# Optimization experiments

Measured on AMD Instinct MI355X. Metric: run time of the kernel, lower is better.

Reference implementation:

```python
import jax, jax.numpy as jnp
import numpy as np
import math

H = 8  # num_heads
SCALE = 1.0 / math.sqrt(512.0)  # original divides by sqrt(dim_V), not sqrt(head_dim)


def setup_inputs() -> dict:
    key = jax.random.key(0)
    ks = jax.random.split(key, 16)
    B, N, D = 32, 512, 512
    s = 1.0 / math.sqrt(D)
    return {
        "Q": jax.random.normal(ks[0], (B, N, D), jnp.float32),
        "K": jax.random.normal(ks[1], (B, N, D), jnp.float32),
        "Wq": jax.random.normal(ks[2], (D, D), jnp.float32) * s,
        "bq": jnp.zeros((D,), jnp.float32),
        "Wk": jax.random.normal(ks[3], (D, D), jnp.float32) * s,
        "bk": jnp.zeros((D,), jnp.float32),
        "Wv": jax.random.normal(ks[4], (D, D), jnp.float32) * s,
        "bv": jnp.zeros((D,), jnp.float32),
        "Wo": jax.random.normal(ks[5], (D, D), jnp.float32) * s,
        "bo": jnp.zeros((D,), jnp.float32),
        "W1": jax.random.normal(ks[6], (D, D), jnp.float32) * s,
        "b1": jnp.zeros((D,), jnp.float32),
        "W2": jax.random.normal(ks[7], (D, D), jnp.float32) * s,
        "b2": jnp.zeros((D,), jnp.float32),
    }


def reference(Q, K, Wq, bq, Wk, bk, Wv, bv, Wo, bo, W1, b1, W2, b2):
    B, Nq, D = Q.shape
    dh = D // H
    # projections (torch Linear: x @ W.T + b)
    q = (Q @ Wq.T + bq).reshape(B, Nq, H, dh)
    k = (K @ Wk.T + bk).reshape(B, K.shape[1], H, dh)
    v = (K @ Wv.T + bv).reshape(B, K.shape[1], H, dh)
    # scores: [B, H, Nq, Nk], scaled by 1/sqrt(dim_V)
    scores = jnp.einsum("bqhd,bkhd->bhqk", q, k) * SCALE
    # NOTE: original softmax is over dim=1 of [H*B, Nq, Nk] == the QUERY axis
    A = jax.nn.softmax(scores, axis=2)
    attn = jnp.einsum("bhqk,bkhd->bqhd", A, v).reshape(B, Nq, D)
    out = Q + (attn @ Wo.T + bo)  # dropout p=0.0
    ffn = jax.nn.relu(out @ W1.T + b1) @ W2.T + b2
    return out + ffn
```

## Files before the change

kernel.cpp:

```cpp
#include <hip/hip_runtime.h>
#include <stdint.h>

#define SCALE_ 0.044194173824159216f

typedef __attribute__((ext_vector_type(8))) short bf16x8;
typedef __attribute__((ext_vector_type(4))) float f32x4;

__device__ __forceinline__ ushort f2b(float f) {
  union { float f; uint32_t u; } v; v.f = f;
  return (ushort)((v.u + 0x7fffu + ((v.u >> 16) & 1u)) >> 16);
}
__device__ __forceinline__ uint32_t cvtpk(float lo, float hi) {
  uint32_t r; asm("v_cvt_pk_bf16_f32 %0, %1, %2" : "=v"(r) : "v"(lo), "v"(hi)); return r;
}
__device__ __forceinline__ void gld16(void* lds, const void* g) {
  __builtin_amdgcn_global_load_lds(
      (const __attribute__((address_space(1))) uint32_t*)g,
      (__attribute__((address_space(3))) uint32_t*)lds, 16, 0, 0);
}

__global__ __launch_bounds__(256)
void k_cvt(const float* __restrict__ Q, const float* __restrict__ K,
           const float* __restrict__ w0, const float* __restrict__ w1,
           const float* __restrict__ w2, const float* __restrict__ w3,
           const float* __restrict__ w4, const float* __restrict__ w5,
           ushort* __restrict__ Qb, ushort* __restrict__ Kb, ushort* __restrict__ Wb)
{
  const long long NQ = 8388608LL, NW = 262144LL;
  long long i = ((long long)blockIdx.x * 256 + threadIdx.x) * 4;
  const float* src; ushort* dst; long long off;
  if (i < NQ)        { src = Q; dst = Qb; off = i; }
  else if (i < 2*NQ) { src = K; dst = Kb; off = i - NQ; }
  else {
    long long j = i - 2*NQ; int seg = (int)(j / NW); off = j - (long long)seg * NW;
    switch (seg) { case 0: src = w0; break; case 1: src = w1; break; case 2: src = w2; break;
                   case 3: src = w3; break; case 4: src = w4; break; default: src = w5; }
    dst = Wb + (size_t)seg * NW;
  }
  float4 v = *(const float4*)(src + off);
  ushort4 o = make_ushort4(f2b(v.x), f2b(v.y), f2b(v.z), f2b(v.w));
  *(ushort4*)(dst + off) = o;
}

template<int EPI>
__device__ __forceinline__ void gemm_body(const ushort* __restrict__ A, const ushort* __restrict__ Bw,
                                          const float* __restrict__ bias, const float* __restrict__ extra,
                                          float* __restrict__ outf, ushort* __restrict__ outb,
                                          char* lds, int m0, int n0)
{
  const int t = threadIdx.x;
  const int w = t >> 6, lane = t & 63;
  const int wm = w >> 1, wn = w & 1;
  const int rA = lane & 15, g = lane >> 4;

  const ushort* srcA[4]; int ldsA[4];
#pragma unroll
  for (int j = 0; j < 4; j++) {
    int L = (t + j*512) * 16;
    int U = L ^ (((L >> 7) & 7) << 4);
    srcA[j] = A + (size_t)(m0 + (U >> 7))*512 + ((U & 127) >> 1);
    ldsA[j] = L;
  }
  const ushort* srcB[2]; int ldsB[2];
#pragma unroll
  for (int j = 0; j < 2; j++) {
    int L = (t + j*512) * 16;
    int U = L ^ (((L >> 7) & 7) << 4);
    srcB[j] = Bw + (size_t)(n0 + (U >> 7))*512 + ((U & 127) >> 1);
    ldsB[j] = 32768 + L;
  }

#define STAGE(ti) do { \
    char* bb_ = lds + ((ti) % 3) * 49152; \
    _Pragma("unroll") \
    for (int j = 0; j < 4; j++) gld16(bb_ + ldsA[j], srcA[j] + (ti)*64); \
    _Pragma("unroll") \
    for (int j = 0; j < 2; j++) gld16(bb_ + ldsB[j], srcB[j] + (ti)*64); } while (0)

  STAGE(0);
  STAGE(1);

  f32x4 acc[4][4] = {};
  for (int i = 0; i < 8; i++) {
    if (i < 7) asm volatile("s_waitcnt vmcnt(6)" ::: "memory");
    else       asm volatile("s_waitcnt vmcnt(0)" ::: "memory");
    __builtin_amdgcn_s_barrier();
    __builtin_amdgcn_sched_barrier(0);
    if (i < 6) STAGE(i + 2);
    const char* bufc = lds + (i % 3) * 49152;
#pragma unroll
    for (int ks = 0; ks < 2; ks++) {
      bf16x8 af[4], bfr[4];
#pragma unroll
      for (int m = 0; m < 4; m++) {
        int row = wm*64 + m*16 + rA;
        int off = (row*128 + ks*64 + g*16) ^ ((row & 7) << 4);
        af[m] = *(const bf16x8*)(bufc + off);
      }
#pragma unroll
      for (int n = 0; n < 4; n++) {
        int row = wn*64 + n*16 + rA;
        int off = 32768 + ((row*128 + ks*64 + g*16) ^ ((row & 7) << 4));
        bfr[n] = *(const bf16x8*)(bufc + off);
      }
      __builtin_amdgcn_s_setprio(1);
#pragma unroll
      for (int m = 0; m < 4; m++)
#pragma unroll
        for (int n = 0; n < 4; n++)
          acc[m][n] = __builtin_amdgcn_mfma_f32_16x16x32_bf16(af[m], bfr[n], acc[m][n], 0, 0, 0);
      __builtin_amdgcn_s_setprio(0);
    }
  }
#undef STAGE

#pragma unroll
  for (int m = 0; m < 4; m++)
#pragma unroll
    for (int n = 0; n < 4; n++) {
      int col = n0 + wn*64 + n*16 + rA;
      float bb = bias[col];
      if (EPI == 4) {
        int b = m0 >> 9, k0 = m0 & 511;
        int hh = col >> 6, dl = col & 63;
        int kg = k0 + wm*64 + m*16 + g*4;
        float v0 = acc[m][n][0] + bb, v1 = acc[m][n][1] + bb;
        float v2 = acc[m][n][2] + bb, v3 = acc[m][n][3] + bb;
        uint2 pk;
        pk.x = (uint32_t)f2b(v0) | ((uint32_t)f2b(v1) << 16);
        pk.y = (uint32_t)f2b(v2) | ((uint32_t)f2b(v3) << 16);
        *(uint2*)(outb + ((size_t)((b*8 + hh)*64 + dl)*512 + kg)) = pk;
      } else {
#pragma unroll
        for (int r = 0; r < 4; r++) {
          int row = m0 + wm*64 + m*16 + g*4 + r;
          size_t idx = (size_t)row*512 + col;
          float v = acc[m][n][r] + bb;
          if (EPI == 0)      outb[idx] = f2b(v);
          else if (EPI == 1) { float o = extra[idx] + v; outf[idx] = o; outb[idx] = f2b(o); }
          else if (EPI == 2) outb[idx] = f2b(v > 0.f ? v : 0.f);
          else               outf[idx] += v;
        }
      }
    }
}

template<int EPI>
__global__ __launch_bounds__(512, 2)
void k_gemm(const ushort* __restrict__ A, const ushort* __restrict__ Bw,
            const float* __restrict__ bias, const float* __restrict__ extra,
            float* __restrict__ outf, ushort* __restrict__ outb)
{
  __shared__ __align__(16) char lds[3*49152];
  gemm_body<EPI>(A, Bw, bias, extra, outf, outb, lds, blockIdx.x*256, blockIdx.y*128);
}

__global__ __launch_bounds__(512, 2)
void k_gemm_qkv(const ushort* __restrict__ Qb, const ushort* __restrict__ Kb,
                const ushort* __restrict__ Wb, const float* __restrict__ bq,
                const float* __restrict__ bk, const float* __restrict__ bvv,
                ushort* __restrict__ qkout, ushort* __restrict__ vpT)
{
  __shared__ __align__(16) char lds[3*49152];
  int z = blockIdx.z;
  if (z == 2) {
    gemm_body<4>(Kb, Wb + 2*(size_t)262144, bvv, nullptr, nullptr,
                 vpT, lds, blockIdx.x*256, blockIdx.y*128);
  } else {
    const ushort* A = (z == 0) ? Qb : Kb;
    const float* bias = (z == 0) ? bq : bk;
    gemm_body<0>(A, Wb + (size_t)z*262144, bias, nullptr, nullptr,
                 qkout + (size_t)z*8388608, lds, blockIdx.x*256, blockIdx.y*128);
  }
}

__global__ __launch_bounds__(256, 2)
void k_z(const ushort* __restrict__ qp, const ushort* __restrict__ kp, float* __restrict__ zinv)
{
  __shared__ __align__(16) ushort qt[2*8192];
  int bid = blockIdx.x;
  int bh = bid >> 1, kh = bid & 1;
  int b = bh >> 3, h = bh & 7;
  int t = threadIdx.x, w = t >> 6, lane = t & 63;
  int rA = lane & 15, g = lane >> 4;
  const ushort* qbase = qp + (size_t)(b*512)*512 + h*64;
  bf16x8 kf[4][2];
#pragma unroll
  for (int n = 0; n < 4; n++)
#pragma unroll
    for (int ks = 0; ks < 2; ks++)
      kf[n][ks] = *(const bf16x8*)(kp + (size_t)(b*512 + kh*256 + w*64 + n*16 + rA)*512 + h*64 + ks*32 + g*8);

#define Z_STAGE(buf, qb) do { \
    _Pragma("unroll") \
    for (int i = 0; i < 4; i++) { \
      int c = i*256 + w*64 + lane; \
      int row = c >> 3, sl = c & 7; \
      gld16((char*)qt + (buf)*16384 + i*4096 + w*1024, \
            qbase + (size_t)((qb)*128 + row)*512 + ((sl ^ (row & 7))*8)); } } while (0)

  Z_STAGE(0, 0);
  __syncthreads();
  float Zacc[4] = {0.f, 0.f, 0.f, 0.f};
  for (int qb = 0; qb < 4; qb++) {
    const int cur = qb & 1;
    if (qb < 3) Z_STAGE(cur ^ 1, qb + 1);
    const ushort* qtb = qt + cur*8192;
    f32x4 acc[8][4] = {};
#pragma unroll
    for (int ks = 0; ks < 2; ks++) {
      bf16x8 af[8];
#pragma unroll
      for (int m = 0; m < 8; m++) {
        int q = m*16 + rA;
        af[m] = *(const bf16x8*)(qtb + q*64 + (((ks*4 + g) ^ (q & 7))*8));
      }
      __builtin_amdgcn_s_setprio(1);
#pragma unroll
      for (int m = 0; m < 8; m++)
#pragma unroll
        for (int n = 0; n < 4; n++)
          acc[m][n] = __builtin_amdgcn_mfma_f32_16x16x32_bf16(af[m], kf[n][ks], acc[m][n], 0, 0, 0);
      __builtin_amdgcn_s_setprio(0);
    }
#pragma unroll
    for (int m = 0; m < 8; m++)
#pragma unroll
      for (int n = 0; n < 4; n++) {
        float s = 0.f;
#pragma unroll
        for (int r = 0; r < 4; r++) s += __expf(acc[m][n][r] * SCALE_);
        Zacc[n] += s;
      }
    __syncthreads();
  }
#undef Z_STAGE
#pragma unroll
  for (int n = 0; n < 4; n++) {
    float v = Zacc[n];
    v += __shfl_xor(v, 16);
    v += __shfl_xor(v, 32);
    if (lane < 16) zinv[(size_t)bh*512 + kh*256 + w*64 + n*16 + lane] = 1.0f / v;
  }
}

__global__ __launch_bounds__(256, 2)
void k_attn(const ushort* __restrict__ qp, const ushort* __restrict__ kp,
            const ushort* __restrict__ vpT, const float* __restrict__ zinv,
            ushort* __restrict__ attn)
{
  __shared__ __align__(16) ushort kt2[2*4096];
  __shared__ __align__(16) ushort vt2[2*4096];
  __shared__ __align__(16) ushort P[4*4096];
  __shared__ float zl[512];
  int bid = blockIdx.x;
  int bh = bid >> 1, qh = bid & 1;
  int b = bh >> 3, h = bh & 7;
  int t = threadIdx.x, w = t >> 6, lane = t & 63;
  int rA = lane & 15, g = lane >> 4;
  const ushort* kbase = kp + (size_t)(b*512)*512 + h*64;
  const ushort* vbase = vpT + (size_t)bh*64*512;
  ushort* Pw = P + w*4096;
  bf16x8 qf[4][2];
#pragma unroll
  for (int m = 0; m < 4; m++)
#pragma unroll
    for (int ks = 0; ks < 2; ks++)
      qf[m][ks] = *(const bf16x8*)(qp + (size_t)(b*512 + qh*256 + w*64 + m*16 + rA)*512 + h*64 + ks*32 + g*8);

#define A_STAGE(buf, kc) do { \
    _Pragma("unroll") \
    for (int i = 0; i < 2; i++) { \
      int c = i*256 + w*64 + lane; \
      { int k = c >> 3, sl = c & 7; \
        gld16((char*)kt2 + (buf)*8192 + i*4096 + w*1024, \
              kbase + (size_t)((kc)*64 + k)*512 + ((sl ^ (k & 7))*8)); } \
      { int d = c >> 3, sl = c & 7; \
        gld16((char*)vt2 + (buf)*8192 + i*4096 + w*1024, \
              vbase + (size_t)d*512 + (kc)*64 + ((sl ^ (d & 7))*8)); } } } while (0)

  A_STAGE(0, 0);
  zl[t]       = zinv[(size_t)bh*512 + t];
  zl[t + 256] = zinv[(size_t)bh*512 + t + 256];
  __syncthreads();
  f32x4 oacc[4][4] = {};
  for (int kc = 0; kc < 8; kc++) {
    const int cur = kc & 1;
    if (kc < 7) A_STAGE(cur ^ 1, kc + 1);
    const ushort* ktb = kt2 + cur*4096;
    const ushort* vtb = vt2 + cur*4096;
#pragma unroll
    for (int knh = 0; knh < 2; knh++) {
      f32x4 sacc[2][4] = {};
#pragma unroll
      for (int ks = 0; ks < 2; ks++) {
        bf16x8 kfr[2];
#pragma unroll
        for (int kn2 = 0; kn2 < 2; kn2++) {
          int k = (knh*2 + kn2)*16 + rA;
          kfr[kn2] = *(const bf16x8*)(ktb + k*64 + (((ks*4 + g) ^ (k & 7))*8));
        }
        __builtin_amdgcn_s_setprio(1);
#pragma unroll
        for (int kn2 = 0; kn2 < 2; kn2++)
#pragma unroll
          for (int m = 0; m < 4; m++)
            sacc[kn2][m] = __builtin_amdgcn_mfma_f32_16x16x32_bf16(kfr[kn2], qf[m][ks], sacc[kn2][m], 0, 0, 0);
        __builtin_amdgcn_s_setprio(0);
      }
#pragma unroll
      for (int kn2 = 0; kn2 < 2; kn2++) {
        int kn = knh*2 + kn2;
        f32x4 zv = *(const f32x4*)&zl[kc*64 + kn*16 + g*4];
#pragma unroll
        for (int m = 0; m < 4; m++) {
          float e0 = __expf(sacc[kn2][m][0] * SCALE_) * zv[0];
          float e1 = __expf(sacc[kn2][m][1] * SCALE_) * zv[1];
          float e2 = __expf(sacc[kn2][m][2] * SCALE_) * zv[2];
          float e3 = __expf(sacc[kn2][m][3] * SCALE_) * zv[3];
          uint2 pk; pk.x = cvtpk(e0, e1); pk.y = cvtpk(e2, e3);
          int q = m*16 + rA;
          int kb2 = kn*32 + g*8;
          *(uint2*)((char*)Pw + q*128 + (kb2 ^ ((q & 7) << 4))) = pk;
        }
      }
    }
#pragma unroll
    for (int ks = 0; ks < 2; ks++) {
      bf16x8 pa[4], vb[4];
#pragma unroll
      for (int m = 0; m < 4; m++) {
        int q = m*16 + rA;
        pa[m] = *(const bf16x8*)((const char*)Pw + q*128 + ((ks*64 + g*16) ^ ((q & 7) << 4)));
      }
#pragma unroll
      for (int n = 0; n < 4; n++) {
        int d = n*16 + rA;
        vb[n] = *(const bf16x8*)((const char*)vtb + d*128 + ((ks*64 + g*16) ^ ((d & 7) << 4)));
      }
      __builtin_amdgcn_s_setprio(1);
#pragma unroll
      for (int m = 0; m < 4; m++)
#pragma unroll
        for (int n = 0; n < 4; n++)
          oacc[m][n] = __builtin_amdgcn_mfma_f32_16x16x32_bf16(pa[m], vb[n], oacc[m][n], 0, 0, 0);
      __builtin_amdgcn_s_setprio(0);
    }
    __syncthreads();
  }
#undef A_STAGE
#pragma unroll
  for (int m = 0; m < 4; m++)
#pragma unroll
    for (int n = 0; n < 4; n++)
#pragma unroll
      for (int r = 0; r < 4; r++) {
        int q = qh*256 + w*64 + m*16 + g*4 + r;
        int dcol = h*64 + n*16 + rA;
        attn[(size_t)(b*512 + q)*512 + dcol] = f2b(oacc[m][n][r]);
      }
}

extern "C" void kernel_launch(void* const* d_in, const int* in_sizes, int n_in,
                              void* d_out, int out_size, void* d_ws, size_t ws_size,
                              hipStream_t stream) {
  const float* Q  = (const float*)d_in[0];
  const float* K  = (const float*)d_in[1];
  const float* Wq = (const float*)d_in[2];
  const float* bq = (const float*)d_in[3];
  const float* Wk = (const float*)d_in[4];
  const float* bk = (const float*)d_in[5];
  const float* Wv = (const float*)d_in[6];
  const float* bv = (const float*)d_in[7];
  const float* Wo = (const float*)d_in[8];
  const float* bo = (const float*)d_in[9];
  const float* W1 = (const float*)d_in[10];
  const float* b1 = (const float*)d_in[11];
  const float* W2 = (const float*)d_in[12];
  const float* b2 = (const float*)d_in[13];
  float* out = (float*)d_out;

  const size_t SZ = (size_t)16384 * 512;
  ushort* Qb   = (ushort*)d_ws;
  ushort* Kb   = Qb + SZ;
  ushort* qp   = Kb + SZ;
  ushort* kp   = qp + SZ;
  ushort* vpT  = kp + SZ;
  ushort* Wb   = vpT + SZ;
  float*  zinv = (float*)(Wb + 6 * (size_t)262144);
  ushort* attn = Qb;
  ushort* outb = Kb;
  ushort* h1   = vpT;

  k_cvt<<<dim3(17920), dim3(256), 0, stream>>>(Q, K, Wq, Wk, Wv, Wo, W1, W2, Qb, Kb, Wb);
  k_gemm_qkv<<<dim3(64, 4, 3), dim3(512), 0, stream>>>(Qb, Kb, Wb, bq, bk, bv, qp, vpT);
  k_z<<<dim3(512), dim3(256), 0, stream>>>(qp, kp, zinv);
  k_attn<<<dim3(512), dim3(256), 0, stream>>>(qp, kp, vpT, zinv, attn);
  k_gemm<1><<<dim3(64, 4), dim3(512), 0, stream>>>(attn, Wb + 3*(size_t)262144, bo, Q, out, outb);
  k_gemm<2><<<dim3(64, 4), dim3(512), 0, stream>>>(outb, Wb + 4*(size_t)262144, b1, nullptr, nullptr, h1);
  k_gemm<3><<<dim3(64, 4), dim3(512), 0, stream>>>(h1, Wb + 5*(size_t)262144, b2, nullptr, out, nullptr);
}
```

Before: 164.7 us.

## Split GEMM K-step into two phases interleaving LDS reads, prefetch and MFMA

Restructures the projection GEMM main loop so each k-tile is handled in two half-steps. The A and B global-to-LDS prefetches are issued separately, between the LDS fragment reads, and extra barriers are added to stagger loads against MFMA work. The aim is better overlap of global load issue, LDS reads and matrix instructions, in the style of a ping-pong schedule. The cost is two extra workgroup barriers per iteration and higher register pressure, since both half-step fragment sets are live at once.

```diff
diff --git a/kernel.cpp b/kernel.cpp
--- a/kernel.cpp
+++ b/kernel.cpp
@@ -70,15 +70,15 @@
     ldsB[j] = 32768 + L;
   }
 
-#define STAGE(ti) do { \
-    char* bb_ = lds + ((ti) % 3) * 49152; \
+#define STAGE_A(ti) do { char* bb_ = lds + ((ti) % 3) * 49152; \
     _Pragma("unroll") \
-    for (int j = 0; j < 4; j++) gld16(bb_ + ldsA[j], srcA[j] + (ti)*64); \
+    for (int j = 0; j < 4; j++) gld16(bb_ + ldsA[j], srcA[j] + (ti)*64); } while (0)
+#define STAGE_B(ti) do { char* bb_ = lds + ((ti) % 3) * 49152; \
     _Pragma("unroll") \
     for (int j = 0; j < 2; j++) gld16(bb_ + ldsB[j], srcB[j] + (ti)*64); } while (0)
 
-  STAGE(0);
-  STAGE(1);
+  STAGE_A(0); STAGE_B(0);
+  STAGE_A(1); STAGE_B(1);
 
   f32x4 acc[4][4] = {};
   for (int i = 0; i < 8; i++) {
@@ -86,33 +86,55 @@
     else       asm volatile("s_waitcnt vmcnt(0)" ::: "memory");
     __builtin_amdgcn_s_barrier();
     __builtin_amdgcn_sched_barrier(0);
-    if (i < 6) STAGE(i + 2);
     const char* bufc = lds + (i % 3) * 49152;
-#pragma unroll
-    for (int ks = 0; ks < 2; ks++) {
-      bf16x8 af[4], bfr[4];
-#pragma unroll
-      for (int m = 0; m < 4; m++) {
-        int row = wm*64 + m*16 + rA;
-        int off = (row*128 + ks*64 + g*16) ^ ((row & 7) << 4);
-        af[m] = *(const bf16x8*)(bufc + off);
-      }
-#pragma unroll
-      for (int n = 0; n < 4; n++) {
-        int row = wn*64 + n*16 + rA;
-        int off = 32768 + ((row*128 + ks*64 + g*16) ^ ((row & 7) << 4));
-        bfr[n] = *(const bf16x8*)(bufc + off);
-      }
-      __builtin_amdgcn_s_setprio(1);
-#pragma unroll
-      for (int m = 0; m < 4; m++)
-#pragma unroll
-        for (int n = 0; n < 4; n++)
-          acc[m][n] = __builtin_amdgcn_mfma_f32_16x16x32_bf16(af[m], bfr[n], acc[m][n], 0, 0, 0);
-      __builtin_amdgcn_s_setprio(0);
-    }
-  }
-#undef STAGE
+
+    bf16x8 afA[4], bfA[4];
+#pragma unroll
+    for (int m = 0; m < 4; m++) {
+      int row = wm*64 + m*16 + rA;
+      afA[m] = *(const bf16x8*)(bufc + ((row*128 + g*16) ^ ((row & 7) << 4)));
+    }
+#pragma unroll
+    for (int n = 0; n < 4; n++) {
+      int row = wn*64 + n*16 + rA;
+      bfA[n] = *(const bf16x8*)(bufc + 32768 + ((row*128 + g*16) ^ ((row & 7) << 4)));
+    }
+    if (i < 6) STAGE_A(i + 2);
+    __builtin_amdgcn_s_barrier();
+    __builtin_amdgcn_sched_barrier(0);
+
+    bf16x8 afB[4], bfB[4];
+#pragma unroll
+    for (int m = 0; m < 4; m++) {
+      int row = wm*64 + m*16 + rA;
+      afB[m] = *(const bf16x8*)(bufc + ((row*128 + 64 + g*16) ^ ((row & 7) << 4)));
+    }
+#pragma unroll
+    for (int n = 0; n < 4; n++) {
+      int row = wn*64 + n*16 + rA;
+      bfB[n] = *(const bf16x8*)(bufc + 32768 + ((row*128 + 64 + g*16) ^ ((row & 7) << 4)));
+    }
+    if (i < 6) STAGE_B(i + 2);
+    __builtin_amdgcn_s_setprio(1);
+#pragma unroll
+    for (int m = 0; m < 4; m++)
+#pragma unroll
+      for (int n = 0; n < 4; n++)
+        acc[m][n] = __builtin_amdgcn_mfma_f32_16x16x32_bf16(afA[m], bfA[n], acc[m][n], 0, 0, 0);
+    __builtin_amdgcn_s_setprio(0);
+    __builtin_amdgcn_s_barrier();
+    __builtin_amdgcn_sched_barrier(0);
+
+    __builtin_amdgcn_s_setprio(1);
+#pragma unroll
+    for (int m = 0; m < 4; m++)
+#pragma unroll
+      for (int n = 0; n < 4; n++)
+        acc[m][n] = __builtin_amdgcn_mfma_f32_16x16x32_bf16(afB[m], bfB[n], acc[m][n], 0, 0, 0);
+    __builtin_amdgcn_s_setprio(0);
+  }
+#undef STAGE_A
+#undef STAGE_B
 
 #pragma unroll
   for (int m = 0; m < 4; m++)
```

Result: no change. 164.9 us (+0.1%).
